# Kernel tuning notes

Measured on AMD Instinct MI355X. Metric: run time of the kernel, lower is better.

Reference implementation:

```python
import jax, jax.numpy as jnp
import numpy as np

N_VIEW = 100      # hardcoded n_view in _hard_anchor_sampling
TEMP = 20.0       # self.temperature
BASE_TEMP = 0.1   # self.base_temperature


def _sample_one(x, yh, yp, key):
    # x: [N, D] flattened spatial features, yh = labels, yp = predict (flattened)
    N = yh.shape[0]
    ar = jnp.arange(N)
    hard_mask = (yh == 0) & (yp == 0)            # (y_hat==0)&(y==0)
    easy_mask = (yh == 1) & (yp == 1)            # (y_hat==1)&(y==1)
    # torch keeps the first 50 hard nonzero indices (randperm over range(50) only permutes them)
    hard_idx = jnp.argsort(jnp.where(hard_mask, ar, N))[:N_VIEW // 2]
    # torch keeps a random 50-subset of the easy positives (randperm sampling)
    scores = jnp.where(easy_mask, jax.random.uniform(key, (N,)), -1.0)
    _, easy_idx = jax.lax.top_k(scores, N_VIEW // 2)
    # X_[ii, 0:50] = easy, X_[ii, 50:100] = hard
    return jnp.concatenate([x[easy_idx], x[hard_idx]], axis=0)  # [100, D]


def _contrastive(X_):
    # X_: [2, 100, D]; torch.cat(torch.unbind(X_, dim=1), dim=0) interleaves views-major
    A = jnp.swapaxes(X_, 0, 1).reshape(2 * N_VIEW, -1)  # [200, D]
    # F.normalize (contrast_feature is the same normalized anchor in the source)
    A = A / jnp.maximum(jnp.linalg.norm(A, axis=1, keepdims=True), 1e-12)
    logits = (A @ A.T) / BASE_TEMP
    logits = logits - jax.lax.stop_gradient(jnp.max(logits, axis=1, keepdims=True))
    idx = jnp.arange(2 * N_VIEW)
    # mask = kron([[1,0],[0,1]], ones(100,100)) -> 100x100 block diagonal
    mask0 = (idx[:, None] // N_VIEW == idx[None, :] // N_VIEW).astype(logits.dtype)
    neg_mask = 1.0 - mask0  # computed BEFORE logits_mask is applied
    # scatter_(1, arange(100).view(-1,1), 0) on a 200x200 tensor only zeros the
    # diagonal of the first 100 rows
    r = jnp.arange(N_VIEW)
    logits_mask = jnp.ones_like(mask0).at[r, r].set(0.0)
    mask = mask0 * logits_mask
    exp_l = jnp.exp(logits)
    neg = (exp_l * neg_mask).sum(axis=1, keepdims=True)
    log_prob = jnp.log(exp_l / (exp_l + neg))
    mean_lpp = (log_prob * mask).sum(axis=1) / mask.sum(axis=1)
    return -(mean_lpp / TEMP).mean()


def _forward(feats, labels, predict):
    B, D = feats.shape[0], feats.shape[1]
    x = jnp.moveaxis(feats, 1, -1).reshape(B, -1, D)  # [B, N, D]
    yh = labels.reshape(B, -1)
    yp = predict.reshape(B, -1)
    keys = jax.random.split(jax.random.key(42), B)
    X_ = jax.vmap(_sample_one)(x, yh, yp, keys)       # [2, 100, D]
    return _contrastive(X_)


def setup_inputs() -> dict:
    key = jax.random.key(0)
    k1, k2, k3 = jax.random.split(key, 3)
    feats = jax.random.normal(k1, (2, 128, 32, 64, 64), dtype=jnp.float32)
    labels = jax.random.randint(k2, (2, 32, 64, 64), 0, 2)
    predict = jax.random.randint(k3, (2, 32, 64, 64), 0, 2)
    return {"feats": feats, "labels": labels, "predict": predict}


def reference(feats, labels, predict):
    return _forward(feats, labels, predict)
```

## Files before the change

### kernel.cpp

```cpp
#include <hip/hip_runtime.h>
#include <stdint.h>

#define NPIX   131072
#define HALFN  65536
#define KSEL   50
#define CAP_E  1024
#define CAP_H  2048
#define THR    0.99f
#define CSTR   32
#define SENT_HARD 0xFFFFFFFFu
#define SENT_NONE 0xFFFFFFFEu

__host__ __device__ __forceinline__ uint32_t rotl32(uint32_t v, int d) {
  return (v << d) | (v >> (32 - d));
}

__host__ __device__ __forceinline__ void tf_block(uint32_t k0, uint32_t k1,
                                                  uint32_t c0, uint32_t c1,
                                                  uint32_t& o0, uint32_t& o1) {
  uint32_t ks2 = k0 ^ k1 ^ 0x1BD11BDAu;
  uint32_t x0 = c0 + k0, x1 = c1 + k1;
#define TF_R(r) { x0 += x1; x1 = rotl32(x1, (r)); x1 ^= x0; }
  TF_R(13) TF_R(15) TF_R(26) TF_R(6)   x0 += k1;  x1 += ks2 + 1u;
  TF_R(17) TF_R(29) TF_R(16) TF_R(24)  x0 += ks2; x1 += k0  + 2u;
  TF_R(13) TF_R(15) TF_R(26) TF_R(6)   x0 += k0;  x1 += k1  + 3u;
  TF_R(17) TF_R(29) TF_R(16) TF_R(24)  x0 += k1;  x1 += ks2 + 4u;
  TF_R(13) TF_R(15) TF_R(26) TF_R(6)   x0 += ks2; x1 += k0  + 5u;
#undef TF_R
  o0 = x0; o1 = x1;
}

__global__ void k_zero(int* cnts, float* out) {
  int i = threadIdx.x;
  if (i < 8 * CSTR) cnts[i] = 0;
  if (i == 0) out[0] = 0.f;
}

__global__ __launch_bounds__(512) void k_scores(
    const int* __restrict__ labels, const int* __restrict__ predict,
    uint32_t* __restrict__ scores, uint64_t* __restrict__ ecand,
    uint32_t* __restrict__ hcand, int* __restrict__ cnts,
    uint32_t k00, uint32_t k01, uint32_t k10, uint32_t k11) {
  int gid = blockIdx.x * blockDim.x + threadIdx.x;
  int b = gid >> 17;
  int n = gid & (NPIX - 1);
  int tid = threadIdx.x, wv = tid >> 6, lane = tid & 63;
  int yh = labels[gid], yp = predict[gid];
  bool is_easy = (yh == 1 && yp == 1);
  bool is_hard = (yh == 0 && yp == 0);
  uint32_t sval = SENT_NONE;
  float u = -1.f;
  if (is_easy) {
    uint32_t ka = b ? k10 : k00, kb = b ? k11 : k01;
    uint32_t o0, o1, bits;
    if (n < HALFN) { tf_block(ka, kb, (uint32_t)n, (uint32_t)(n + HALFN), o0, o1); bits = o0; }
    else           { tf_block(ka, kb, (uint32_t)(n - HALFN), (uint32_t)n, o0, o1); bits = o1; }
    u = __uint_as_float((bits >> 9) | 0x3F800000u) - 1.0f;
    sval = __float_as_uint(u);
  } else if (is_hard) {
    sval = SENT_HARD;
  }
  scores[gid] = sval;

  bool cand_e = is_easy && (u >= THR);
  bool cand_h = is_hard && (n < CAP_H);
  uint64_t bal_e  = __ballot(is_easy), bal_h  = __ballot(is_hard);
  uint64_t bal_ec = __ballot(cand_e),  bal_hc = __ballot(cand_h);

  __shared__ int we[8], wh[8], wec[8], whc[8];
  __shared__ int base_ec, base_hc;
  if (lane == 0) {
    we[wv]  = __popcll(bal_e);  wh[wv]  = __popcll(bal_h);
    wec[wv] = __popcll(bal_ec); whc[wv] = __popcll(bal_hc);
  }
  __syncthreads();
  if (tid == 0) {
    int te = 0, th = 0, tec = 0, thc = 0;
    for (int w = 0; w < 8; ++w) { te += we[w]; th += wh[w]; tec += wec[w]; thc += whc[w]; }
    if (te) atomicAdd(&cnts[(b * 4 + 0) * CSTR], te);
    if (th) atomicAdd(&cnts[(b * 4 + 2) * CSTR], th);
    base_ec = tec ? atomicAdd(&cnts[(b * 4 + 1) * CSTR], tec) : 0;
    base_hc = thc ? atomicAdd(&cnts[(b * 4 + 3) * CSTR], thc) : 0;
  }
  __syncthreads();
  if (cand_e) {
    int pre = 0;
    for (int w = 0; w < wv; ++w) pre += wec[w];
    int p = base_ec + pre + __popcll(bal_ec & ((1ull << lane) - 1));
    if (p < CAP_E)
      ecand[b * CAP_E + p] = ((uint64_t)sval << 32) | (uint32_t)(~(uint32_t)n);
  }
  if (cand_h) {
    int pre = 0;
    for (int w = 0; w < wv; ++w) pre += whc[w];
    int p = base_hc + pre + __popcll(bal_hc & ((1ull << lane) - 1));
    hcand[b * CAP_H + p] = (uint32_t)n;
  }
}

__global__ __launch_bounds__(1024) void k_select(const uint32_t* __restrict__ scores,
                                                 const uint64_t* __restrict__ ecand,
                                                 const uint32_t* __restrict__ hcand,
                                                 const int* __restrict__ cnts,
                                                 int* __restrict__ easy_out,
                                                 int* __restrict__ hard_out) {
  int b = blockIdx.x;
  int tid = threadIdx.x;
  int wv = tid >> 6, lane = tid & 63;
  __shared__ uint64_t se[CAP_E];
  __shared__ uint32_t shd[CAP_H];
  __shared__ uint64_t wred[16];
  __shared__ uint64_t s_win;

  int et = cnts[(b * 4 + 0) * CSTR], ec = cnts[(b * 4 + 1) * CSTR];
  int ht = cnts[(b * 4 + 2) * CSTR], hc = cnts[(b * 4 + 3) * CSTR];
  int eneed = et < KSEL ? et : KSEL;
  int hneed = ht < KSEL ? ht : KSEL;
  bool fast_easy = (ec <= CAP_E) && (ec >= eneed);
  bool fast_hard = (hc >= hneed);

  if (fast_easy) {
    se[tid] = (tid < ec) ? ecand[b * CAP_E + tid] : 0ull;
    __syncthreads();
    for (int k2 = 2; k2 <= CAP_E; k2 <<= 1) {
      for (int j = k2 >> 1; j > 0; j >>= 1) {
        int ixj = tid ^ j;
        if (ixj > tid) {
          uint64_t a = se[tid], c = se[ixj];
          bool asc = ((tid & k2) == 0);
          if (asc ? (a > c) : (a < c)) { se[tid] = c; se[ixj] = a; }
        }
        __syncthreads();
      }
    }
    int take = ec < KSEL ? ec : KSEL;
    if (tid < take) easy_out[b * 64 + tid] = (int)(~(uint32_t)se[CAP_E - 1 - tid]);
    __syncthreads();
    if (tid == 0 && take < KSEL) {
      int slot = take;
      for (int n = 0; n < NPIX && slot < KSEL; ++n)
        if (scores[b * NPIX + n] >= SENT_NONE) easy_out[b * 64 + slot++] = n;
    }
    __syncthreads();
  } else {
    uint64_t prev = 0xFFFFFFFFFFFFFFFFull;
    int k = 0;
    for (; k < KSEL; ++k) {
      uint64_t lmax = 0;
      for (int i = tid; i < NPIX; i += 1024) {
        uint32_t v = scores[b * NPIX + i];
        if (v < SENT_NONE) {
          uint64_t key = ((uint64_t)v << 32) | (uint32_t)(~(uint32_t)i);
          if (key < prev && key > lmax) lmax = key;
        }
      }
      for (int off = 32; off; off >>= 1) {
        uint64_t o = __shfl_down(lmax, off);
        if (o > lmax) lmax = o;
      }
      if (lane == 0) wred[wv] = lmax;
      __syncthreads();
      if (tid == 0) {
        uint64_t m = 0;
        for (int w = 0; w < 16; ++w) if (wred[w] > m) m = wred[w];
        s_win = m;
      }
      __syncthreads();
      uint64_t win = s_win;
      __syncthreads();
      if (win == 0) break;
      if (tid == 0) easy_out[b * 64 + k] = (int)(~(uint32_t)win);
      prev = win;
    }
    if (tid == 0 && k < KSEL) {
      int slot = k;
      for (int n = 0; n < NPIX && slot < KSEL; ++n)
        if (scores[b * NPIX + n] >= SENT_NONE) easy_out[b * 64 + slot++] = n;
    }
    __syncthreads();
  }

  if (fast_hard) {
    for (int m = tid; m < CAP_H; m += 1024)
      shd[m] = (m < hc) ? hcand[b * CAP_H + m] : 0xFFFFFFFFu;
    __syncthreads();
    for (int k2 = 2; k2 <= CAP_H; k2 <<= 1) {
      for (int j = k2 >> 1; j > 0; j >>= 1) {
        for (int m = tid; m < CAP_H; m += 1024) {
          int ixj = m ^ j;
          if (ixj > m) {
            uint32_t a = shd[m], c = shd[ixj];
            bool asc = ((m & k2) == 0);
            if (asc ? (a > c) : (a < c)) { shd[m] = c; shd[ixj] = a; }
          }
        }
        __syncthreads();
      }
    }
    int take = hc < KSEL ? hc : KSEL;
    if (tid < take) hard_out[b * 64 + tid] = (int)shd[tid];
    __syncthreads();
    if (tid == 0 && take < KSEL) {
      int slot = take;
      for (int n = 0; n < NPIX && slot < KSEL; ++n)
        if (scores[b * NPIX + n] != SENT_HARD) hard_out[b * 64 + slot++] = n;
    }
    __syncthreads();
  } else {
    int prev = -1;
    int k = 0;
    for (; k < KSEL; ++k) {
      uint32_t lmin = 0xFFFFFFFFu;
      for (int i = tid; i < NPIX; i += 1024) {
        uint32_t v = scores[b * NPIX + i];
        if (v == SENT_HARD && i > prev && (uint32_t)i < lmin) lmin = (uint32_t)i;
      }
      for (int off = 32; off; off >>= 1) {
        uint32_t o = (uint32_t)__shfl_down(lmin, off);
        if (o < lmin) lmin = o;
      }
      if (lane == 0) wred[wv] = lmin;
      __syncthreads();
      if (tid == 0) {
        uint32_t m = 0xFFFFFFFFu;
        for (int w = 0; w < 16; ++w) if ((uint32_t)wred[w] < m) m = (uint32_t)wred[w];
        s_win = m;
      }
      __syncthreads();
      uint32_t win = (uint32_t)s_win;
      __syncthreads();
      if (win == 0xFFFFFFFFu) break;
      if (tid == 0) hard_out[b * 64 + k] = (int)win;
      prev = (int)win;
    }
    if (tid == 0 && k < KSEL) {
      int slot = k;
      for (int n = 0; n < NPIX && slot < KSEL; ++n)
        if (scores[b * NPIX + n] != SENT_HARD) hard_out[b * 64 + slot++] = n;
    }
    __syncthreads();
  }
}

__global__ void k_gather(const float* __restrict__ feats, const int* __restrict__ easy_out,
                         const int* __restrict__ hard_out, float* __restrict__ A) {
  int r = blockIdx.x;
  int d = threadIdx.x;
  int v = r & 1, i = r >> 1;
  int n = (i < KSEL) ? easy_out[v * 64 + i] : hard_out[v * 64 + (i - KSEL)];
  float val = feats[((size_t)(v * 128 + d)) * NPIX + (size_t)n];
  float sq = val * val;
  for (int off = 32; off; off >>= 1) sq += __shfl_down(sq, off);
  __shared__ float wsum[2];
  __shared__ float s_inv;
  if ((d & 63) == 0) wsum[d >> 6] = sq;
  __syncthreads();
  if (d == 0) s_inv = 1.0f / fmaxf(sqrtf(wsum[0] + wsum[1]), 1e-12f);
  __syncthreads();
  A[r * 128 + d] = val * s_inv;
}

__global__ __launch_bounds__(256) void k_loss(const float* __restrict__ A,
                                              float* __restrict__ out) {
  int r = blockIdx.x;
  int c = threadIdx.x;
  __shared__ float arow[128];
  __shared__ float red[256];
  if (c < 128) arow[c] = A[r * 128 + c];
  __syncthreads();
  bool valid = c < 200;
  float logit = -1e30f;
  if (valid) {
    const float* Ac = A + c * 128;
    float dot = 0.f;
#pragma unroll 8
    for (int d = 0; d < 128; ++d) dot += arow[d] * Ac[d];
    logit = dot * 10.0f;
  }
  red[c] = logit;
  __syncthreads();
  for (int s = 128; s; s >>= 1) { if (c < s) { float o = red[c + s]; if (o > red[c]) red[c] = o; } __syncthreads(); }
  float M = red[0];
  __syncthreads();
  float e = valid ? expf(logit - M) : 0.f;
  bool sameblk = valid && ((r / 100) == (c / 100));
  red[c] = (valid && !sameblk) ? e : 0.f;
  __syncthreads();
  for (int s = 128; s; s >>= 1) { if (c < s) red[c] += red[c + s]; __syncthreads(); }
  float neg = red[0];
  __syncthreads();
  bool msk = sameblk && !(r < 100 && c == r);
  red[c] = msk ? ((logit - M) - logf(e + neg)) : 0.f;
  __syncthreads();
  for (int s = 128; s; s >>= 1) { if (c < s) red[c] += red[c + s]; __syncthreads(); }
  if (c == 0) {
    float denom = (r < 100) ? 99.f : 100.f;
    atomicAdd(out, -(red[0] / denom) / (20.0f * 200.0f));
  }
}

extern "C" void kernel_launch(void* const* d_in, const int* in_sizes, int n_in,
                              void* d_out, int out_size, void* d_ws, size_t ws_size,
                              hipStream_t stream) {
  const float* feats  = (const float*)d_in[0];
  const int* labels   = (const int*)d_in[1];
  const int* predict  = (const int*)d_in[2];
  float* out = (float*)d_out;

  char* ws = (char*)d_ws;
  uint32_t* scores = (uint32_t*)ws;
  uint64_t* ecand  = (uint64_t*)(ws + (size_t)2 * NPIX * 4);
  uint32_t* hcand  = (uint32_t*)((char*)ecand + 2 * CAP_E * 8);
  int* cnts  = (int*)((char*)hcand + 2 * CAP_H * 4);
  int* easy  = cnts + 8 * CSTR;
  int* hard  = easy + 2 * 64;
  float* A   = (float*)(hard + 2 * 64);

  uint32_t a0, a1, b0, b1;
  tf_block(0u, 42u, 0u, 2u, a0, a1);
  tf_block(0u, 42u, 1u, 3u, b0, b1);

  k_zero<<<1, 256, 0, stream>>>(cnts, out);
  k_scores<<<(2 * NPIX) / 512, 512, 0, stream>>>(labels, predict, scores, ecand, hcand, cnts, a0, b0, a1, b1);
  k_select<<<2, 1024, 0, stream>>>(scores, ecand, hcand, cnts, easy, hard);
  k_gather<<<200, 128, 0, stream>>>(feats, easy, hard, A);
  k_loss<<<200, 256, 0, stream>>>(A, out);
}
```

Measured before the change: 216.0 us.

## Fuse selection into gather with per-row rank counting instead of bitonic sort

Removes the two-block k_select kernel and merges selection into the 200-block gather kernel. Each block finds its own selected index, using a rank count over the shared-memory candidate list in place of a full bitonic sort, and then gathers and normalizes that feature row. This spreads selection across many blocks and drops one launch plus the easy/hard index buffers. In exchange, every block redundantly loads and ranks the whole candidate list with O(n^2) comparisons, and the fallback scan paths become far costlier per block.

```diff
diff --git a/kernel.cpp b/kernel.cpp
--- a/kernel.cpp
+++ b/kernel.cpp
@@ -98,166 +98,151 @@
   }
 }
 
-__global__ __launch_bounds__(1024) void k_select(const uint32_t* __restrict__ scores,
-                                                 const uint64_t* __restrict__ ecand,
-                                                 const uint32_t* __restrict__ hcand,
-                                                 const int* __restrict__ cnts,
-                                                 int* __restrict__ easy_out,
-                                                 int* __restrict__ hard_out) {
-  int b = blockIdx.x;
+__device__ __forceinline__ bool cond_eval(uint32_t s, int cid) {
+  return cid == 0 ? (s >= SENT_NONE) : (cid == 1 ? (s == SENT_HARD) : (s != SENT_HARD));
+}
+
+__device__ int nth_min_pred(const uint32_t* __restrict__ sc, int want, int cid,
+                            int tid, int lane, int wv, uint32_t* s_w32, int* foundcnt) {
+  int prev = -1;
+  int k = 0;
+  for (; k <= want; ++k) {
+    uint32_t lmin = 0xFFFFFFFFu;
+    for (int m = tid; m < NPIX; m += 128) {
+      if (cond_eval(sc[m], cid) && m > prev && (uint32_t)m < lmin) lmin = (uint32_t)m;
+    }
+    for (int off = 32; off; off >>= 1) {
+      uint32_t o = (uint32_t)__shfl_down(lmin, off);
+      if (o < lmin) lmin = o;
+    }
+    if (lane == 0) s_w32[wv] = lmin;
+    __syncthreads();
+    uint32_t g = s_w32[0] < s_w32[1] ? s_w32[0] : s_w32[1];
+    __syncthreads();
+    if (g == 0xFFFFFFFFu) break;
+    prev = (int)g;
+  }
+  *foundcnt = k;
+  return prev;
+}
+
+__global__ __launch_bounds__(128) void k_selgather(
+    const uint32_t* __restrict__ scores, const uint64_t* __restrict__ ecand,
+    const uint32_t* __restrict__ hcand, const int* __restrict__ cnts,
+    const float* __restrict__ feats, float* __restrict__ A) {
+  int r = blockIdx.x;
   int tid = threadIdx.x;
-  int wv = tid >> 6, lane = tid & 63;
+  int lane = tid & 63, wv = tid >> 6;
+  int v = r & 1, i = r >> 1;
+  int b = v;
+  const uint32_t* sc = scores + (size_t)b * NPIX;
+
   __shared__ uint64_t se[CAP_E];
   __shared__ uint32_t shd[CAP_H];
-  __shared__ uint64_t wred[16];
-  __shared__ uint64_t s_win;
+  __shared__ uint32_t s_w32[2];
+  __shared__ uint64_t s_w64[2];
+  __shared__ int s_n;
 
   int et = cnts[(b * 4 + 0) * CSTR], ec = cnts[(b * 4 + 1) * CSTR];
   int ht = cnts[(b * 4 + 2) * CSTR], hc = cnts[(b * 4 + 3) * CSTR];
-  int eneed = et < KSEL ? et : KSEL;
-  int hneed = ht < KSEL ? ht : KSEL;
-  bool fast_easy = (ec <= CAP_E) && (ec >= eneed);
-  bool fast_hard = (hc >= hneed);
-
-  if (fast_easy) {
-    se[tid] = (tid < ec) ? ecand[b * CAP_E + tid] : 0ull;
-    __syncthreads();
-    for (int k2 = 2; k2 <= CAP_E; k2 <<= 1) {
-      for (int j = k2 >> 1; j > 0; j >>= 1) {
-        int ixj = tid ^ j;
-        if (ixj > tid) {
-          uint64_t a = se[tid], c = se[ixj];
-          bool asc = ((tid & k2) == 0);
-          if (asc ? (a > c) : (a < c)) { se[tid] = c; se[ixj] = a; }
+
+  if (i < KSEL) {
+    int eneed = et < KSEL ? et : KSEL;
+    bool fast = (ec <= CAP_E) && (ec >= eneed);
+    if (fast) {
+      int take = ec < KSEL ? ec : KSEL;
+      if (i < take) {
+        for (int t = tid; t < ec; t += 128) se[t] = ecand[b * CAP_E + t];
+        __syncthreads();
+        for (int t = tid; t < ec; t += 128) {
+          uint64_t mine = se[t];
+          int rank = 0;
+          for (int j = 0; j < ec; ++j) rank += (se[j] > mine);
+          if (rank == i) s_n = (int)(~(uint32_t)mine);
         }
         __syncthreads();
-      }
-    }
-    int take = ec < KSEL ? ec : KSEL;
-    if (tid < take) easy_out[b * 64 + tid] = (int)(~(uint32_t)se[CAP_E - 1 - tid]);
-    __syncthreads();
-    if (tid == 0 && take < KSEL) {
-      int slot = take;
-      for (int n = 0; n < NPIX && slot < KSEL; ++n)
-        if (scores[b * NPIX + n] >= SENT_NONE) easy_out[b * 64 + slot++] = n;
-    }
-    __syncthreads();
-  } else {
-    uint64_t prev = 0xFFFFFFFFFFFFFFFFull;
-    int k = 0;
-    for (; k < KSEL; ++k) {
-      uint64_t lmax = 0;
-      for (int i = tid; i < NPIX; i += 1024) {
-        uint32_t v = scores[b * NPIX + i];
-        if (v < SENT_NONE) {
-          uint64_t key = ((uint64_t)v << 32) | (uint32_t)(~(uint32_t)i);
-          if (key < prev && key > lmax) lmax = key;
-        }
-      }
-      for (int off = 32; off; off >>= 1) {
-        uint64_t o = __shfl_down(lmax, off);
-        if (o > lmax) lmax = o;
-      }
-      if (lane == 0) wred[wv] = lmax;
-      __syncthreads();
-      if (tid == 0) {
-        uint64_t m = 0;
-        for (int w = 0; w < 16; ++w) if (wred[w] > m) m = wred[w];
-        s_win = m;
-      }
-      __syncthreads();
-      uint64_t win = s_win;
-      __syncthreads();
-      if (win == 0) break;
-      if (tid == 0) easy_out[b * 64 + k] = (int)(~(uint32_t)win);
-      prev = win;
-    }
-    if (tid == 0 && k < KSEL) {
-      int slot = k;
-      for (int n = 0; n < NPIX && slot < KSEL; ++n)
-        if (scores[b * NPIX + n] >= SENT_NONE) easy_out[b * 64 + slot++] = n;
-    }
-    __syncthreads();
-  }
-
-  if (fast_hard) {
-    for (int m = tid; m < CAP_H; m += 1024)
-      shd[m] = (m < hc) ? hcand[b * CAP_H + m] : 0xFFFFFFFFu;
-    __syncthreads();
-    for (int k2 = 2; k2 <= CAP_H; k2 <<= 1) {
-      for (int j = k2 >> 1; j > 0; j >>= 1) {
-        for (int m = tid; m < CAP_H; m += 1024) {
-          int ixj = m ^ j;
-          if (ixj > m) {
-            uint32_t a = shd[m], c = shd[ixj];
-            bool asc = ((m & k2) == 0);
-            if (asc ? (a > c) : (a < c)) { shd[m] = c; shd[ixj] = a; }
+      } else {
+        int fc;
+        int nsel = nth_min_pred(sc, i - take, 0, tid, lane, wv, s_w32, &fc);
+        if (tid == 0) s_n = nsel;
+        __syncthreads();
+      }
+    } else {
+      uint64_t prev = 0xFFFFFFFFFFFFFFFFull;
+      int found = 0, nsel = -1;
+      for (int k = 0; k <= i; ++k) {
+        uint64_t lmax = 0;
+        for (int m = tid; m < NPIX; m += 128) {
+          uint32_t s = sc[m];
+          if (s < SENT_NONE) {
+            uint64_t key = ((uint64_t)s << 32) | (uint32_t)(~(uint32_t)m);
+            if (key < prev && key > lmax) lmax = key;
           }
         }
-        __syncthreads();
-      }
+        for (int off = 32; off; off >>= 1) {
+          uint64_t o = __shfl_down(lmax, off);
+          if (o > lmax) lmax = o;
+        }
+        if (lane == 0) s_w64[wv] = lmax;
+        __syncthreads();
+        uint64_t g = s_w64[0] > s_w64[1] ? s_w64[0] : s_w64[1];
+        __syncthreads();
+        if (g == 0) break;
+        prev = g; found = k + 1;
+        if (k == i) nsel = (int)(~(uint32_t)g);
+      }
+      if (nsel < 0) {
+        int fc;
+        nsel = nth_min_pred(sc, i - found, 0, tid, lane, wv, s_w32, &fc);
+      }
+      if (tid == 0) s_n = nsel;
+      __syncthreads();
     }
-    int take = hc < KSEL ? hc : KSEL;
-    if (tid < take) hard_out[b * 64 + tid] = (int)shd[tid];
-    __syncthreads();
-    if (tid == 0 && take < KSEL) {
-      int slot = take;
-      for (int n = 0; n < NPIX && slot < KSEL; ++n)
-        if (scores[b * NPIX + n] != SENT_HARD) hard_out[b * 64 + slot++] = n;
+  } else {
+    int j = i - KSEL;
+    int hneed = ht < KSEL ? ht : KSEL;
+    bool fast = (hc >= hneed);
+    if (fast) {
+      int take = hc < KSEL ? hc : KSEL;
+      if (j < take) {
+        for (int t = tid; t < hc; t += 128) shd[t] = hcand[b * CAP_H + t];
+        __syncthreads();
+        for (int t = tid; t < hc; t += 128) {
+          uint32_t mine = shd[t];
+          int rank = 0;
+          for (int m = 0; m < hc; ++m) rank += (shd[m] < mine);
+          if (rank == j) s_n = (int)mine;
+        }
+        __syncthreads();
+      } else {
+        int fc;
+        int nsel = nth_min_pred(sc, j - take, 2, tid, lane, wv, s_w32, &fc);
+        if (tid == 0) s_n = nsel;
+        __syncthreads();
+      }
+    } else {
+      int fc = 0;
+      int nsel = nth_min_pred(sc, j, 1, tid, lane, wv, s_w32, &fc);
+      if (fc < j + 1) {
+        int fc2;
+        nsel = nth_min_pred(sc, j - fc, 2, tid, lane, wv, s_w32, &fc2);
+      }
+      if (tid == 0) s_n = nsel;
+      __syncthreads();
     }
-    __syncthreads();
-  } else {
-    int prev = -1;
-    int k = 0;
-    for (; k < KSEL; ++k) {
-      uint32_t lmin = 0xFFFFFFFFu;
-      for (int i = tid; i < NPIX; i += 1024) {
-        uint32_t v = scores[b * NPIX + i];
-        if (v == SENT_HARD && i > prev && (uint32_t)i < lmin) lmin = (uint32_t)i;
-      }
-      for (int off = 32; off; off >>= 1) {
-        uint32_t o = (uint32_t)__shfl_down(lmin, off);
-        if (o < lmin) lmin = o;
-      }
-      if (lane == 0) wred[wv] = lmin;
-      __syncthreads();
-      if (tid == 0) {
-        uint32_t m = 0xFFFFFFFFu;
-        for (int w = 0; w < 16; ++w) if ((uint32_t)wred[w] < m) m = (uint32_t)wred[w];
-        s_win = m;
-      }
-      __syncthreads();
-      uint32_t win = (uint32_t)s_win;
-      __syncthreads();
-      if (win == 0xFFFFFFFFu) break;
-      if (tid == 0) hard_out[b * 64 + k] = (int)win;
-      prev = (int)win;
-    }
-    if (tid == 0 && k < KSEL) {
-      int slot = k;
-      for (int n = 0; n < NPIX && slot < KSEL; ++n)
-        if (scores[b * NPIX + n] != SENT_HARD) hard_out[b * 64 + slot++] = n;
-    }
-    __syncthreads();
-  }
-}
-
-__global__ void k_gather(const float* __restrict__ feats, const int* __restrict__ easy_out,
-                         const int* __restrict__ hard_out, float* __restrict__ A) {
-  int r = blockIdx.x;
-  int d = threadIdx.x;
-  int v = r & 1, i = r >> 1;
-  int n = (i < KSEL) ? easy_out[v * 64 + i] : hard_out[v * 64 + (i - KSEL)];
-  float val = feats[((size_t)(v * 128 + d)) * NPIX + (size_t)n];
+  }
+
+  int n = s_n;
+  float val = feats[((size_t)(v * 128 + tid)) * NPIX + (size_t)n];
   float sq = val * val;
   for (int off = 32; off; off >>= 1) sq += __shfl_down(sq, off);
   __shared__ float wsum[2];
   __shared__ float s_inv;
-  if ((d & 63) == 0) wsum[d >> 6] = sq;
-  __syncthreads();
-  if (d == 0) s_inv = 1.0f / fmaxf(sqrtf(wsum[0] + wsum[1]), 1e-12f);
-  __syncthreads();
-  A[r * 128 + d] = val * s_inv;
+  if (lane == 0) wsum[wv] = sq;
+  __syncthreads();
+  if (tid == 0) s_inv = 1.0f / fmaxf(sqrtf(wsum[0] + wsum[1]), 1e-12f);
+  __syncthreads();
+  A[r * 128 + tid] = val * s_inv;
 }
 
 __global__ __launch_bounds__(256) void k_loss(const float* __restrict__ A,
@@ -312,9 +297,7 @@
   uint64_t* ecand  = (uint64_t*)(ws + (size_t)2 * NPIX * 4);
   uint32_t* hcand  = (uint32_t*)((char*)ecand + 2 * CAP_E * 8);
   int* cnts  = (int*)((char*)hcand + 2 * CAP_H * 4);
-  int* easy  = cnts + 8 * CSTR;
-  int* hard  = easy + 2 * 64;
-  float* A   = (float*)(hard + 2 * 64);
+  float* A   = (float*)(cnts + 8 * CSTR);
 
   uint32_t a0, a1, b0, b1;
   tf_block(0u, 42u, 0u, 2u, a0, a1);
@@ -322,7 +305,6 @@
 
   k_zero<<<1, 256, 0, stream>>>(cnts, out);
   k_scores<<<(2 * NPIX) / 512, 512, 0, stream>>>(labels, predict, scores, ecand, hcand, cnts, a0, b0, a1, b1);
-  k_select<<<2, 1024, 0, stream>>>(scores, ecand, hcand, cnts, easy, hard);
-  k_gather<<<200, 128, 0, stream>>>(feats, easy, hard, A);
+  k_selgather<<<200, 128, 0, stream>>>(scores, ecand, hcand, cnts, feats, A);
   k_loss<<<200, 256, 0, stream>>>(A, out);
 }
```

After: 202.5 us. 6.3% less time.
